# Kernel optimization log

Measured on AMD Instinct MI355X. Metric: run time of the kernel, lower is better.

The kernel has to match this reference:

```python
import jax, jax.numpy as jnp
import numpy as np

N_NODES = 10000
N_EDGES = 160000
NEG_SLOPE = 0.2  # PyG GATConv default leaky_relu slope


def gat_conv(x, src, dst, W, a_src, a_dst, b, heads, out_ch, concat, n):
    # linear projection per head: [n, heads, out_ch]
    h = (x @ W).reshape(n, heads, out_ch)
    # per-node attention logits
    al_s = jnp.sum(h * a_src, axis=-1)  # [n, heads]
    al_d = jnp.sum(h * a_dst, axis=-1)  # [n, heads]
    # per-edge score, softmax over incoming edges of each destination node
    e = jax.nn.leaky_relu(al_s[src] + al_d[dst], NEG_SLOPE)  # [E, heads]
    m = jax.ops.segment_max(e, dst, num_segments=n)
    p = jnp.exp(e - m[dst])
    s = jax.ops.segment_sum(p, dst, num_segments=n)
    alpha = p / (s[dst] + 1e-16)  # [E, heads]
    # weighted scatter-aggregate of source messages
    out = jax.ops.segment_sum(h[src] * alpha[..., None], dst, num_segments=n)
    out = out.reshape(n, heads * out_ch) if concat else out.mean(axis=1)
    return out + b


def setup_inputs() -> dict:
    key = jax.random.key(0)
    ks = jax.random.split(key, 16)
    x = jax.random.normal(ks[0], (N_NODES, 32), dtype=jnp.float32)
    edge_index = jax.random.randint(ks[1], (2, N_EDGES), 0, N_NODES, dtype=jnp.int64)

    def glorot(k, shape):
        fan = shape[0] + shape[-1]
        return jax.random.uniform(k, shape, jnp.float32, -1.0, 1.0) * jnp.sqrt(6.0 / fan)

    # layer 1: 32 -> 8 per head, 8 heads, concat -> 64
    W1 = glorot(ks[2], (32, 64))
    asrc1 = glorot(ks[3], (8, 8))
    adst1 = glorot(ks[4], (8, 8))
    b1 = jnp.zeros((64,), jnp.float32)
    # layer 2: 64 -> 64 per head, 8 heads, concat -> 512
    W2 = glorot(ks[5], (64, 512))
    asrc2 = glorot(ks[6], (8, 64))
    adst2 = glorot(ks[7], (8, 64))
    b2 = jnp.zeros((512,), jnp.float32)
    # layer 3: 512 -> 6, 1 head, no concat
    W3 = glorot(ks[8], (512, 6))
    asrc3 = glorot(ks[9], (1, 6))
    adst3 = glorot(ks[10], (1, 6))
    b3 = jnp.zeros((6,), jnp.float32)

    return dict(x=x, edge_index=edge_index,
                W1=W1, asrc1=asrc1, adst1=adst1, b1=b1,
                W2=W2, asrc2=asrc2, adst2=adst2, b2=b2,
                W3=W3, asrc3=asrc3, adst3=adst3, b3=b3)


def reference(x, edge_index, W1, asrc1, adst1, b1, W2, asrc2, adst2, b2, W3, asrc3, adst3, b3):
    n = x.shape[0]
    # PyG GATConv adds self-loops by default
    loops = jnp.arange(n, dtype=edge_index.dtype)
    src = jnp.concatenate([edge_index[0], loops])
    dst = jnp.concatenate([edge_index[1], loops])
    # dropout layers are identity in eval mode
    h = jax.nn.elu(gat_conv(x, src, dst, W1, asrc1, adst1, b1, 8, 8, True, n))
    h = jax.nn.elu(gat_conv(h, src, dst, W2, asrc2, adst2, b2, 8, 64, True, n))
    out = gat_conv(h, src, dst, W3, asrc3, adst3, b3, 1, 6, False, n)
    return out
```

## Files before the change

### kernel.cpp

```cpp
#include <hip/hip_runtime.h>
#include <hip/hip_bf16.h>
#include <math.h>


#define NEG_SLOPE 0.2f


__global__ __launch_bounds__(256) void count_deg(const int* __restrict__ ei,
                                                 int* __restrict__ deg, int E) {
  int e = blockIdx.x * blockDim.x + threadIdx.x;
  if (e < E) atomicAdd(&deg[ei[E + e]], 1);
}

__global__ __launch_bounds__(1024) void scan_k(const int* __restrict__ deg,
                                               int* __restrict__ rowptr,
                                               int* __restrict__ cursor, int n) {
  __shared__ int part[1024];
  int t = threadIdx.x;
  int chunk = (n + 1023) >> 10;
  int lo = t * chunk;
  int hi = min(lo + chunk, n);
  int s = 0;
  for (int i = lo; i < hi; ++i) s += deg[i];
  part[t] = s;
  __syncthreads();
  for (int off = 1; off < 1024; off <<= 1) {
    int v = (t >= off) ? part[t - off] : 0;
    __syncthreads();
    part[t] += v;
    __syncthreads();
  }
  int run = (t == 0) ? 0 : part[t - 1];
  for (int i = lo; i < hi; ++i) {
    rowptr[i] = run;
    cursor[i] = run;
    run += deg[i];
  }
  if (t == 1023) rowptr[n] = part[1023];
}

__global__ __launch_bounds__(256) void fill_edges(const int* __restrict__ ei,
                                                  int* __restrict__ cursor,
                                                  int* __restrict__ esrc,
                                                  int* __restrict__ edst, int E) {
  int e = blockIdx.x * blockDim.x + threadIdx.x;
  if (e < E) {
    int d = ei[E + e];
    int pos = atomicAdd(&cursor[d], 1);
    esrc[pos] = ei[e];
    edst[pos] = d;
  }
}


__global__ __launch_bounds__(512) void prep_av(const float* __restrict__ W1,
                                               const float* __restrict__ as1,
                                               const float* __restrict__ ad1,
                                               const float* __restrict__ W2,
                                               const float* __restrict__ as2,
                                               const float* __restrict__ ad2,
                                               float* __restrict__ av) {
  int t = threadIdx.x;
  if (blockIdx.x == 0) {
    if (t < 256) {
      int h = t >> 5, k = t & 31;
      float s = 0.f, d = 0.f;
#pragma unroll
      for (int c = 0; c < 8; ++c) {
        float w = W1[k * 64 + h * 8 + c];
        s += w * as1[h * 8 + c];
        d += w * ad1[h * 8 + c];
      }
      av[t] = s;
      av[256 + t] = d;
    }
  } else {
    int h = t >> 6, k = t & 63;
    float s = 0.f, d = 0.f;
#pragma unroll
    for (int c = 0; c < 64; ++c) {
      float w = W2[k * 512 + h * 64 + c];
      s += w * as2[h * 64 + c];
      d += w * ad2[h * 64 + c];
    }
    av[512 + t] = s;
    av[1024 + t] = d;
  }
}


template <int HH, int K>
__global__ __launch_bounds__(256) void logits_x(const float* __restrict__ X,
                                                const float* __restrict__ avs,
                                                const float* __restrict__ avd,
                                                float* __restrict__ als,
                                                float* __restrict__ ald,
                                                float* __restrict__ selfe, int n) {
  int idx = blockIdx.x * blockDim.x + threadIdx.x;
  if (idx >= n * HH) return;
  int node = idx / HH;
  int h = idx - node * HH;
  const float* xr = X + (size_t)node * K;
  const float* vs = avs + h * K;
  const float* vd = avd + h * K;
  float s0 = 0.f, s1 = 0.f;
#pragma unroll
  for (int k4 = 0; k4 < K / 4; ++k4) {
    float4 xv = *reinterpret_cast<const float4*>(&xr[k4 * 4]);
    float4 a = *reinterpret_cast<const float4*>(&vs[k4 * 4]);
    float4 b = *reinterpret_cast<const float4*>(&vd[k4 * 4]);
    s0 += xv.x * a.x + xv.y * a.y + xv.z * a.z + xv.w * a.w;
    s1 += xv.x * b.x + xv.y * b.y + xv.z * b.z + xv.w * b.w;
  }
  als[idx] = s0;
  ald[idx] = s1;
  float e = s0 + s1;
  selfe[idx] = e > 0.f ? e : NEG_SLOPE * e;
}


__global__ __launch_bounds__(256) void logits_h3(const float* __restrict__ HF,
                                                 const float* __restrict__ Asrc,
                                                 const float* __restrict__ Adst,
                                                 float* __restrict__ als,
                                                 float* __restrict__ ald,
                                                 float* __restrict__ selfe, int n) {
  int node = blockIdx.x * blockDim.x + threadIdx.x;
  if (node >= n) return;
  const float* f = HF + (size_t)node * 6;
  float s0 = 0.f, s1 = 0.f;
#pragma unroll
  for (int c = 0; c < 6; ++c) {
    float v = f[c];
    s0 += v * Asrc[c];
    s1 += v * Adst[c];
  }
  als[node] = s0;
  ald[node] = s1;
  float e = s0 + s1;
  selfe[node] = e > 0.f ? e : NEG_SLOPE * e;
}


template <int HH>
__global__ __launch_bounds__(256) void edge_e(const int* __restrict__ esrc,
                                              const int* __restrict__ edst,
                                              const float* __restrict__ als,
                                              const float* __restrict__ ald,
                                              float* __restrict__ evt, int E) {
  int e = blockIdx.x * blockDim.x + threadIdx.x;
  if (e >= E) return;
  int s = esrc[e], d = edst[e];
  if constexpr (HH == 8) {
    float4 s0 = *reinterpret_cast<const float4*>(&als[(size_t)s * 8]);
    float4 s1 = *reinterpret_cast<const float4*>(&als[(size_t)s * 8 + 4]);
    float4 d0 = *reinterpret_cast<const float4*>(&ald[(size_t)d * 8]);
    float4 d1 = *reinterpret_cast<const float4*>(&ald[(size_t)d * 8 + 4]);
    float v[8] = {s0.x + d0.x, s0.y + d0.y, s0.z + d0.z, s0.w + d0.w,
                  s1.x + d1.x, s1.y + d1.y, s1.z + d1.z, s1.w + d1.w};
    float4 o0, o1;
    o0.x = v[0] > 0.f ? v[0] : NEG_SLOPE * v[0];
    o0.y = v[1] > 0.f ? v[1] : NEG_SLOPE * v[1];
    o0.z = v[2] > 0.f ? v[2] : NEG_SLOPE * v[2];
    o0.w = v[3] > 0.f ? v[3] : NEG_SLOPE * v[3];
    o1.x = v[4] > 0.f ? v[4] : NEG_SLOPE * v[4];
    o1.y = v[5] > 0.f ? v[5] : NEG_SLOPE * v[5];
    o1.z = v[6] > 0.f ? v[6] : NEG_SLOPE * v[6];
    o1.w = v[7] > 0.f ? v[7] : NEG_SLOPE * v[7];
    *reinterpret_cast<float4*>(&evt[(size_t)e * 8]) = o0;
    *reinterpret_cast<float4*>(&evt[(size_t)e * 8 + 4]) = o1;
  } else {
    float v = als[s] + ald[d];
    evt[e] = v > 0.f ? v : NEG_SLOPE * v;
  }
}


template <int HH>
__global__ __launch_bounds__(256) void msum_alpha(float* __restrict__ evt,
                                                  const float* __restrict__ selfe,
                                                  const int* __restrict__ rowptr,
                                                  float* __restrict__ asel, int n) {
  int idx = blockIdx.x * blockDim.x + threadIdx.x;
  if (idx >= n * HH) return;
  int node = idx / HH;
  int h = idx - node * HH;
  int r0 = rowptr[node], r1 = rowptr[node + 1];
  float e0 = selfe[idx];
  float m = e0;
  for (int p = r0; p < r1; ++p) m = fmaxf(m, evt[(size_t)p * HH + h]);
  float s = __expf(e0 - m);
  float a0 = s;
  for (int p = r0; p < r1; ++p) s += __expf(evt[(size_t)p * HH + h] - m);
  float rs = 1.f / (s + 1e-16f);
  asel[idx] = a0 * rs;
  for (int p = r0; p < r1; ++p) {
    size_t q = (size_t)p * HH + h;
    evt[q] = __expf(evt[q] - m) * rs;
  }
}


__global__ __launch_bounds__(256) void agg1(const float* __restrict__ X,
                                            const float* __restrict__ alpha,
                                            const float* __restrict__ asel,
                                            const int* __restrict__ rowptr,
                                            const int* __restrict__ esrc,
                                            float* __restrict__ AGG, int n) {
  int node = blockIdx.x * 4 + (threadIdx.x >> 6);
  int lane = threadIdx.x & 63;
  if (node >= n) return;
  int ch = lane & 31;
  int half = lane >> 5;
  float xs = X[((unsigned)node << 5) + ch];
  float acc0 = asel[node * 8 + half * 4 + 0] * xs;
  float acc1 = asel[node * 8 + half * 4 + 1] * xs;
  float acc2 = asel[node * 8 + half * 4 + 2] * xs;
  float acc3 = asel[node * 8 + half * 4 + 3] * xs;
  int r0 = rowptr[node], r1 = rowptr[node + 1];
  int p = r0;
  for (; p + 2 <= r1; p += 2) {
    int s0 = esrc[p], s1 = esrc[p + 1];
    float xv0 = X[((unsigned)s0 << 5) + ch];
    float xv1 = X[((unsigned)s1 << 5) + ch];
    float4 a0 = *reinterpret_cast<const float4*>(&alpha[(size_t)p * 8 + half * 4]);
    float4 a1 = *reinterpret_cast<const float4*>(&alpha[(size_t)(p + 1) * 8 + half * 4]);
    acc0 += a0.x * xv0; acc1 += a0.y * xv0; acc2 += a0.z * xv0; acc3 += a0.w * xv0;
    acc0 += a1.x * xv1; acc1 += a1.y * xv1; acc2 += a1.z * xv1; acc3 += a1.w * xv1;
  }
  if (p < r1) {
    int s0 = esrc[p];
    float xv0 = X[((unsigned)s0 << 5) + ch];
    float4 a0 = *reinterpret_cast<const float4*>(&alpha[(size_t)p * 8 + half * 4]);
    acc0 += a0.x * xv0; acc1 += a0.y * xv0; acc2 += a0.z * xv0; acc3 += a0.w * xv0;
  }
  unsigned base = (unsigned)node * 256 + (unsigned)half * 128 + ch;
  AGG[base] = acc0;
  AGG[base + 32] = acc1;
  AGG[base + 64] = acc2;
  AGG[base + 96] = acc3;
}

__global__ __launch_bounds__(256) void agg2(const float* __restrict__ X,
                                            const float* __restrict__ alpha,
                                            const float* __restrict__ asel,
                                            const int* __restrict__ rowptr,
                                            const int* __restrict__ esrc,
                                            float* __restrict__ AGG, int n) {
  int node = blockIdx.x * 4 + (threadIdx.x >> 6);
  int lane = threadIdx.x & 63;
  if (node >= n) return;
  float acc[8];
  float xs = X[((unsigned)node << 6) + lane];
#pragma unroll
  for (int h = 0; h < 8; ++h) acc[h] = asel[node * 8 + h] * xs;
  int r0 = rowptr[node], r1 = rowptr[node + 1];
  int p = r0;
  for (; p + 2 <= r1; p += 2) {
    int s0 = esrc[p], s1 = esrc[p + 1];
    float xv0 = X[((unsigned)s0 << 6) + lane];
    float xv1 = X[((unsigned)s1 << 6) + lane];
    float4 a00 = *reinterpret_cast<const float4*>(&alpha[(size_t)p * 8]);
    float4 a01 = *reinterpret_cast<const float4*>(&alpha[(size_t)p * 8 + 4]);
    float4 a10 = *reinterpret_cast<const float4*>(&alpha[(size_t)(p + 1) * 8]);
    float4 a11 = *reinterpret_cast<const float4*>(&alpha[(size_t)(p + 1) * 8 + 4]);
    acc[0] += a00.x * xv0; acc[1] += a00.y * xv0;
    acc[2] += a00.z * xv0; acc[3] += a00.w * xv0;
    acc[4] += a01.x * xv0; acc[5] += a01.y * xv0;
    acc[6] += a01.z * xv0; acc[7] += a01.w * xv0;
    acc[0] += a10.x * xv1; acc[1] += a10.y * xv1;
    acc[2] += a10.z * xv1; acc[3] += a10.w * xv1;
    acc[4] += a11.x * xv1; acc[5] += a11.y * xv1;
    acc[6] += a11.z * xv1; acc[7] += a11.w * xv1;
  }
  if (p < r1) {
    int s0 = esrc[p];
    float xv0 = X[((unsigned)s0 << 6) + lane];
    float4 a00 = *reinterpret_cast<const float4*>(&alpha[(size_t)p * 8]);
    float4 a01 = *reinterpret_cast<const float4*>(&alpha[(size_t)p * 8 + 4]);
    acc[0] += a00.x * xv0; acc[1] += a00.y * xv0;
    acc[2] += a00.z * xv0; acc[3] += a00.w * xv0;
    acc[4] += a01.x * xv0; acc[5] += a01.y * xv0;
    acc[6] += a01.z * xv0; acc[7] += a01.w * xv0;
  }
  unsigned base = (unsigned)node * 512 + lane;
#pragma unroll
  for (int h = 0; h < 8; ++h) AGG[base + h * 64] = acc[h];
}


__global__ __launch_bounds__(256) void proj1(const float* __restrict__ AGG,
                                             const float* __restrict__ W1,
                                             const float* __restrict__ b1,
                                             float* __restrict__ OUT, int n) {
  int w = blockIdx.x * 4 + (threadIdx.x >> 6);
  int lane = threadIdx.x & 63;
  int node0 = w * 8;
  if (node0 >= n) return;
  int h = lane >> 3;
  float acc[8];
#pragma unroll
  for (int j = 0; j < 8; ++j) acc[j] = 0.f;
  for (int k = 0; k < 32; ++k) {
    float wv = W1[k * 64 + lane];
#pragma unroll
    for (int j = 0; j < 8; ++j) {
      int nd = min(node0 + j, n - 1);
      acc[j] += AGG[(unsigned)nd * 256 + h * 32 + k] * wv;
    }
  }
  float bv = b1[lane];
#pragma unroll
  for (int j = 0; j < 8; ++j) {
    int nd = node0 + j;
    if (nd >= n) break;
    float v = acc[j] + bv;
    v = v > 0.f ? v : expm1f(v);
    OUT[(unsigned)nd * 64 + lane] = v;
  }
}

__global__ __launch_bounds__(256) void proj2(const float* __restrict__ AGG,
                                             const float* __restrict__ W2,
                                             const float* __restrict__ b2,
                                             float* __restrict__ OUT, int n) {
  int w = blockIdx.x * 4 + (threadIdx.x >> 6);
  int lane = threadIdx.x & 63;
  int node0 = w * 4;
  if (node0 >= n) return;
  int c0 = lane * 8;
  int h = lane >> 3;
  float acc[4][8];
#pragma unroll
  for (int j = 0; j < 4; ++j)
#pragma unroll
    for (int c = 0; c < 8; ++c) acc[j][c] = 0.f;
  for (int k = 0; k < 64; ++k) {
    const float4 w0 = *reinterpret_cast<const float4*>(&W2[(size_t)k * 512 + c0]);
    const float4 w1 = *reinterpret_cast<const float4*>(&W2[(size_t)k * 512 + c0 + 4]);
#pragma unroll
    for (int j = 0; j < 4; ++j) {
      int nd = min(node0 + j, n - 1);
      float xv = AGG[(unsigned)nd * 512 + h * 64 + k];
      acc[j][0] += xv * w0.x; acc[j][1] += xv * w0.y;
      acc[j][2] += xv * w0.z; acc[j][3] += xv * w0.w;
      acc[j][4] += xv * w1.x; acc[j][5] += xv * w1.y;
      acc[j][6] += xv * w1.z; acc[j][7] += xv * w1.w;
    }
  }
  float4 bv0 = *reinterpret_cast<const float4*>(&b2[c0]);
  float4 bv1 = *reinterpret_cast<const float4*>(&b2[c0 + 4]);
#pragma unroll
  for (int j = 0; j < 4; ++j) {
    int nd = node0 + j;
    if (nd >= n) break;
    float v[8];
    v[0] = acc[j][0] + bv0.x; v[1] = acc[j][1] + bv0.y;
    v[2] = acc[j][2] + bv0.z; v[3] = acc[j][3] + bv0.w;
    v[4] = acc[j][4] + bv1.x; v[5] = acc[j][5] + bv1.y;
    v[6] = acc[j][6] + bv1.z; v[7] = acc[j][7] + bv1.w;
#pragma unroll
    for (int c = 0; c < 8; ++c) v[c] = v[c] > 0.f ? v[c] : expm1f(v[c]);
    float4* o = reinterpret_cast<float4*>(&OUT[(unsigned)nd * 512 + c0]);
    o[0] = make_float4(v[0], v[1], v[2], v[3]);
    o[1] = make_float4(v[4], v[5], v[6], v[7]);
  }
}

__global__ __launch_bounds__(64) void gemm_l3(const float* __restrict__ X,
                                              const float* __restrict__ W,
                                              float* __restrict__ H, int n) {
  int node = blockIdx.x;
  int lane = threadIdx.x;
  if (node >= n) return;
  float acc[6] = {0.f, 0.f, 0.f, 0.f, 0.f, 0.f};
  for (int k = lane; k < 512; k += 64) {
    float xv = X[(size_t)node * 512 + k];
#pragma unroll
    for (int c = 0; c < 6; ++c) acc[c] += xv * W[k * 6 + c];
  }
#pragma unroll
  for (int c = 0; c < 6; ++c) {
    float v = acc[c];
    for (int off = 32; off >= 1; off >>= 1) v += __shfl_down(v, off, 64);
    if (lane == 0) H[(size_t)node * 6 + c] = v;
  }
}

__global__ __launch_bounds__(256) void agg_l3(const float* __restrict__ HF,
                                              const float* __restrict__ alpha,
                                              const float* __restrict__ asel,
                                              const float* __restrict__ bias,
                                              const int* __restrict__ rowptr,
                                              const int* __restrict__ esrc,
                                              float* __restrict__ OUT, int n) {
  int node = blockIdx.x * 4 + (threadIdx.x >> 6);
  int lane = threadIdx.x & 63;
  if (node >= n) return;
  int ch = lane < 6 ? lane : 0;
  float acc = asel[node] * HF[(unsigned)node * 6u + ch];
  int r0 = rowptr[node], r1 = rowptr[node + 1];
  int p = r0;
  for (; p + 2 <= r1; p += 2) {
    int s0 = esrc[p], s1 = esrc[p + 1];
    float h0 = HF[(unsigned)s0 * 6u + ch];
    float h1 = HF[(unsigned)s1 * 6u + ch];
    float a0 = alpha[p], a1 = alpha[p + 1];
    acc += a0 * h0 + a1 * h1;
  }
  if (p < r1) acc += alpha[p] * HF[(unsigned)esrc[p] * 6u + ch];
  if (lane < 6) OUT[(unsigned)node * 6u + lane] = acc + bias[lane];
}


extern "C" void kernel_launch(void* const* d_in, const int* in_sizes, int n_in,
                              void* d_out, int out_size, void* d_ws, size_t ws_size,
                              hipStream_t stream) {
  const float* x     = (const float*)d_in[0];
  const int*   ei    = (const int*)d_in[1];
  const float* W1    = (const float*)d_in[2];
  const float* asrc1 = (const float*)d_in[3];
  const float* adst1 = (const float*)d_in[4];
  const float* b1    = (const float*)d_in[5];
  const float* W2    = (const float*)d_in[6];
  const float* asrc2 = (const float*)d_in[7];
  const float* adst2 = (const float*)d_in[8];
  const float* b2    = (const float*)d_in[9];
  const float* W3    = (const float*)d_in[10];
  const float* asrc3 = (const float*)d_in[11];
  const float* adst3 = (const float*)d_in[12];
  const float* b3    = (const float*)d_in[13];
  float* outf = (float*)d_out;

  const int n = in_sizes[0] / 32;
  const int E = in_sizes[1] / 2;

  char* ws = (char*)d_ws;
  size_t off = 0;
  auto alloc = [&](size_t bytes) {
    size_t o = off;
    off = (off + bytes + 255) & ~(size_t)255;
    return ws + o;
  };
  int* deg     = (int*)alloc((size_t)n * 4);
  int* rowptr  = (int*)alloc((size_t)(n + 1) * 4);
  int* cursor  = (int*)alloc((size_t)n * 4);
  int* esrc    = (int*)alloc((size_t)E * 4);
  int* edst    = (int*)alloc((size_t)E * 4);
  float* evt   = (float*)alloc((size_t)E * 8 * 4);
  float* selfe = (float*)alloc((size_t)n * 8 * 4);
  float* als   = (float*)alloc((size_t)n * 8 * 4);
  float* ald   = (float*)alloc((size_t)n * 8 * 4);
  float* asel  = (float*)alloc((size_t)n * 8 * 4);
  float* av    = (float*)alloc((size_t)1536 * 4);
  float* AGG1  = (float*)alloc((size_t)n * 256 * 4);
  float* x1    = (float*)alloc((size_t)n * 64 * 4);
  float* AGG2  = (float*)alloc((size_t)n * 512 * 4);
  float* x2    = (float*)alloc((size_t)n * 512 * 4);
  float* h3    = (float*)alloc((size_t)n * 6 * 4);

  hipMemsetAsync(deg, 0, (size_t)n * 4, stream);
  count_deg<<<(E + 255) / 256, 256, 0, stream>>>(ei, deg, E);
  scan_k<<<1, 1024, 0, stream>>>(deg, rowptr, cursor, n);
  fill_edges<<<(E + 255) / 256, 256, 0, stream>>>(ei, cursor, esrc, edst, E);
  prep_av<<<2, 512, 0, stream>>>(W1, asrc1, adst1, W2, asrc2, adst2, av);

  logits_x<8, 32><<<(n * 8 + 255) / 256, 256, 0, stream>>>(x, av, av + 256, als, ald, selfe, n);
  edge_e<8><<<(E + 255) / 256, 256, 0, stream>>>(esrc, edst, als, ald, evt, E);
  msum_alpha<8><<<(n * 8 + 255) / 256, 256, 0, stream>>>(evt, selfe, rowptr, asel, n);
  agg1<<<(n + 3) / 4, 256, 0, stream>>>(x, evt, asel, rowptr, esrc, AGG1, n);
  proj1<<<(n / 8 + 3) / 4 + 1, 256, 0, stream>>>(AGG1, W1, b1, x1, n);

  logits_x<8, 64><<<(n * 8 + 255) / 256, 256, 0, stream>>>(x1, av + 512, av + 1024, als, ald, selfe, n);
  edge_e<8><<<(E + 255) / 256, 256, 0, stream>>>(esrc, edst, als, ald, evt, E);
  msum_alpha<8><<<(n * 8 + 255) / 256, 256, 0, stream>>>(evt, selfe, rowptr, asel, n);
  agg2<<<(n + 3) / 4, 256, 0, stream>>>(x1, evt, asel, rowptr, esrc, AGG2, n);
  proj2<<<(n / 4 + 3) / 4 + 1, 256, 0, stream>>>(AGG2, W2, b2, x2, n);

  gemm_l3<<<n, 64, 0, stream>>>(x2, W3, h3, n);
  logits_h3<<<(n + 255) / 256, 256, 0, stream>>>(h3, asrc3, adst3, als, ald, selfe, n);
  edge_e<1><<<(E + 255) / 256, 256, 0, stream>>>(esrc, edst, als, ald, evt, E);
  msum_alpha<1><<<(n + 255) / 256, 256, 0, stream>>>(evt, selfe, rowptr, asel, n);
  agg_l3<<<(n + 3) / 4, 256, 0, stream>>>(h3, evt, asel, b3, rowptr, esrc, outf, n);
}
```

Measured before the change: 313.3 us.

## Fuse edge logits into wave-per-node softmax and merge small setup kernels

```diff
diff --git a/kernel.cpp b/kernel.cpp
--- a/kernel.cpp
+++ b/kernel.cpp
@@ -4,6 +4,10 @@
 
 
 #define NEG_SLOPE 0.2f
+
+__device__ __forceinline__ float lrelu(float v) {
+  return v > 0.f ? v : NEG_SLOPE * v;
+}
 
 
 __global__ __launch_bounds__(256) void count_deg(const int* __restrict__ ei,
@@ -12,56 +16,40 @@
   if (e < E) atomicAdd(&deg[ei[E + e]], 1);
 }
 
-__global__ __launch_bounds__(1024) void scan_k(const int* __restrict__ deg,
-                                               int* __restrict__ rowptr,
-                                               int* __restrict__ cursor, int n) {
-  __shared__ int part[1024];
-  int t = threadIdx.x;
-  int chunk = (n + 1023) >> 10;
-  int lo = t * chunk;
-  int hi = min(lo + chunk, n);
-  int s = 0;
-  for (int i = lo; i < hi; ++i) s += deg[i];
-  part[t] = s;
-  __syncthreads();
-  for (int off = 1; off < 1024; off <<= 1) {
-    int v = (t >= off) ? part[t - off] : 0;
-    __syncthreads();
-    part[t] += v;
-    __syncthreads();
-  }
-  int run = (t == 0) ? 0 : part[t - 1];
-  for (int i = lo; i < hi; ++i) {
-    rowptr[i] = run;
-    cursor[i] = run;
-    run += deg[i];
-  }
-  if (t == 1023) rowptr[n] = part[1023];
-}
-
-__global__ __launch_bounds__(256) void fill_edges(const int* __restrict__ ei,
-                                                  int* __restrict__ cursor,
-                                                  int* __restrict__ esrc,
-                                                  int* __restrict__ edst, int E) {
-  int e = blockIdx.x * blockDim.x + threadIdx.x;
-  if (e < E) {
-    int d = ei[E + e];
-    int pos = atomicAdd(&cursor[d], 1);
-    esrc[pos] = ei[e];
-    edst[pos] = d;
-  }
-}
-
-
-__global__ __launch_bounds__(512) void prep_av(const float* __restrict__ W1,
-                                               const float* __restrict__ as1,
-                                               const float* __restrict__ ad1,
-                                               const float* __restrict__ W2,
-                                               const float* __restrict__ as2,
-                                               const float* __restrict__ ad2,
-                                               float* __restrict__ av) {
+__global__ __launch_bounds__(1024) void scan3(const int* __restrict__ deg,
+                                              int* __restrict__ rowptr,
+                                              int* __restrict__ cursor, int n,
+                                              const float* __restrict__ W1,
+                                              const float* __restrict__ as1,
+                                              const float* __restrict__ ad1,
+                                              const float* __restrict__ W2,
+                                              const float* __restrict__ as2,
+                                              const float* __restrict__ ad2,
+                                              float* __restrict__ av) {
   int t = threadIdx.x;
   if (blockIdx.x == 0) {
+    __shared__ int part[1024];
+    int chunk = (n + 1023) >> 10;
+    int lo = t * chunk;
+    int hi = min(lo + chunk, n);
+    int s = 0;
+    for (int i = lo; i < hi; ++i) s += deg[i];
+    part[t] = s;
+    __syncthreads();
+    for (int off = 1; off < 1024; off <<= 1) {
+      int v = (t >= off) ? part[t - off] : 0;
+      __syncthreads();
+      part[t] += v;
+      __syncthreads();
+    }
+    int run = (t == 0) ? 0 : part[t - 1];
+    for (int i = lo; i < hi; ++i) {
+      rowptr[i] = run;
+      cursor[i] = run;
+      run += deg[i];
+    }
+    if (t == 1023) rowptr[n] = part[1023];
+  } else if (blockIdx.x == 1) {
     if (t < 256) {
       int h = t >> 5, k = t & 31;
       float s = 0.f, d = 0.f;
@@ -75,16 +63,29 @@
       av[256 + t] = d;
     }
   } else {
-    int h = t >> 6, k = t & 63;
-    float s = 0.f, d = 0.f;
-#pragma unroll
-    for (int c = 0; c < 64; ++c) {
-      float w = W2[k * 512 + h * 64 + c];
-      s += w * as2[h * 64 + c];
-      d += w * ad2[h * 64 + c];
-    }
-    av[512 + t] = s;
-    av[1024 + t] = d;
+    if (t < 512) {
+      int h = t >> 6, k = t & 63;
+      float s = 0.f, d = 0.f;
+#pragma unroll
+      for (int c = 0; c < 64; ++c) {
+        float w = W2[k * 512 + h * 64 + c];
+        s += w * as2[h * 64 + c];
+        d += w * ad2[h * 64 + c];
+      }
+      av[512 + t] = s;
+      av[1024 + t] = d;
+    }
+  }
+}
+
+__global__ __launch_bounds__(256) void fill_edges(const int* __restrict__ ei,
+                                                  int* __restrict__ cursor,
+                                                  int* __restrict__ esrc, int E) {
+  int e = blockIdx.x * blockDim.x + threadIdx.x;
+  if (e < E) {
+    int d = ei[E + e];
+    int pos = atomicAdd(&cursor[d], 1);
+    esrc[pos] = ei[e];
   }
 }
 
@@ -115,89 +116,78 @@
   als[idx] = s0;
   ald[idx] = s1;
   float e = s0 + s1;
-  selfe[idx] = e > 0.f ? e : NEG_SLOPE * e;
-}
-
-
-__global__ __launch_bounds__(256) void logits_h3(const float* __restrict__ HF,
-                                                 const float* __restrict__ Asrc,
-                                                 const float* __restrict__ Adst,
-                                                 float* __restrict__ als,
-                                                 float* __restrict__ ald,
-                                                 float* __restrict__ selfe, int n) {
-  int node = blockIdx.x * blockDim.x + threadIdx.x;
+  selfe[idx] = lrelu(e);
+}
+
+
+__global__ __launch_bounds__(256) void msum_alpha8(const int* __restrict__ esrc,
+                                                   const float* __restrict__ als,
+                                                   const float* __restrict__ ald,
+                                                   const float* __restrict__ selfe,
+                                                   const int* __restrict__ rowptr,
+                                                   float* __restrict__ alpha,
+                                                   float* __restrict__ asel, int n) {
+  int node = blockIdx.x * 4 + (threadIdx.x >> 6);
+  int lane = threadIdx.x & 63;
   if (node >= n) return;
-  const float* f = HF + (size_t)node * 6;
-  float s0 = 0.f, s1 = 0.f;
-#pragma unroll
-  for (int c = 0; c < 6; ++c) {
-    float v = f[c];
-    s0 += v * Asrc[c];
-    s1 += v * Adst[c];
-  }
-  als[node] = s0;
-  ald[node] = s1;
-  float e = s0 + s1;
-  selfe[node] = e > 0.f ? e : NEG_SLOPE * e;
-}
-
-
-template <int HH>
-__global__ __launch_bounds__(256) void edge_e(const int* __restrict__ esrc,
-                                              const int* __restrict__ edst,
-                                              const float* __restrict__ als,
-                                              const float* __restrict__ ald,
-                                              float* __restrict__ evt, int E) {
-  int e = blockIdx.x * blockDim.x + threadIdx.x;
-  if (e >= E) return;
-  int s = esrc[e], d = edst[e];
-  if constexpr (HH == 8) {
-    float4 s0 = *reinterpret_cast<const float4*>(&als[(size_t)s * 8]);
-    float4 s1 = *reinterpret_cast<const float4*>(&als[(size_t)s * 8 + 4]);
-    float4 d0 = *reinterpret_cast<const float4*>(&ald[(size_t)d * 8]);
-    float4 d1 = *reinterpret_cast<const float4*>(&ald[(size_t)d * 8 + 4]);
-    float v[8] = {s0.x + d0.x, s0.y + d0.y, s0.z + d0.z, s0.w + d0.w,
-                  s1.x + d1.x, s1.y + d1.y, s1.z + d1.z, s1.w + d1.w};
-    float4 o0, o1;
-    o0.x = v[0] > 0.f ? v[0] : NEG_SLOPE * v[0];
-    o0.y = v[1] > 0.f ? v[1] : NEG_SLOPE * v[1];
-    o0.z = v[2] > 0.f ? v[2] : NEG_SLOPE * v[2];
-    o0.w = v[3] > 0.f ? v[3] : NEG_SLOPE * v[3];
-    o1.x = v[4] > 0.f ? v[4] : NEG_SLOPE * v[4];
-    o1.y = v[5] > 0.f ? v[5] : NEG_SLOPE * v[5];
-    o1.z = v[6] > 0.f ? v[6] : NEG_SLOPE * v[6];
-    o1.w = v[7] > 0.f ? v[7] : NEG_SLOPE * v[7];
-    *reinterpret_cast<float4*>(&evt[(size_t)e * 8]) = o0;
-    *reinterpret_cast<float4*>(&evt[(size_t)e * 8 + 4]) = o1;
-  } else {
-    float v = als[s] + ald[d];
-    evt[e] = v > 0.f ? v : NEG_SLOPE * v;
-  }
-}
-
-
-template <int HH>
-__global__ __launch_bounds__(256) void msum_alpha(float* __restrict__ evt,
-                                                  const float* __restrict__ selfe,
-                                                  const int* __restrict__ rowptr,
-                                                  float* __restrict__ asel, int n) {
-  int idx = blockIdx.x * blockDim.x + threadIdx.x;
-  if (idx >= n * HH) return;
-  int node = idx / HH;
-  int h = idx - node * HH;
+  int i = lane >> 3;
+  int h = lane & 7;
+  float aldv = ald[node * 8 + h];
+  float e0 = selfe[node * 8 + h];
   int r0 = rowptr[node], r1 = rowptr[node + 1];
-  float e0 = selfe[idx];
+
   float m = e0;
-  for (int p = r0; p < r1; ++p) m = fmaxf(m, evt[(size_t)p * HH + h]);
-  float s = __expf(e0 - m);
-  float a0 = s;
-  for (int p = r0; p < r1; ++p) s += __expf(evt[(size_t)p * HH + h] - m);
-  float rs = 1.f / (s + 1e-16f);
-  asel[idx] = a0 * rs;
-  for (int p = r0; p < r1; ++p) {
-    size_t q = (size_t)p * HH + h;
-    evt[q] = __expf(evt[q] - m) * rs;
-  }
+  for (int p = r0 + i; p < r1; p += 8)
+    m = fmaxf(m, lrelu(als[esrc[p] * 8 + h] + aldv));
+  m = fmaxf(m, __shfl_xor(m, 8, 64));
+  m = fmaxf(m, __shfl_xor(m, 16, 64));
+  m = fmaxf(m, __shfl_xor(m, 32, 64));
+
+  float s = 0.f;
+  for (int p = r0 + i; p < r1; p += 8)
+    s += __expf(lrelu(als[esrc[p] * 8 + h] + aldv) - m);
+  s += __shfl_xor(s, 8, 64);
+  s += __shfl_xor(s, 16, 64);
+  s += __shfl_xor(s, 32, 64);
+  float a0 = __expf(e0 - m);
+  float rs = 1.f / (s + a0 + 1e-16f);
+  if (lane < 8) asel[node * 8 + lane] = a0 * rs;
+
+  for (int p = r0 + i; p < r1; p += 8)
+    alpha[(size_t)p * 8 + h] = __expf(lrelu(als[esrc[p] * 8 + h] + aldv) - m) * rs;
+}
+
+__global__ __launch_bounds__(256) void msum_alpha1(const int* __restrict__ esrc,
+                                                   const float* __restrict__ als,
+                                                   const float* __restrict__ ald,
+                                                   const float* __restrict__ selfe,
+                                                   const int* __restrict__ rowptr,
+                                                   float* __restrict__ alpha,
+                                                   float* __restrict__ asel, int n) {
+  int node = blockIdx.x * 4 + (threadIdx.x >> 6);
+  int lane = threadIdx.x & 63;
+  if (node >= n) return;
+  float aldv = ald[node];
+  float e0 = selfe[node];
+  int r0 = rowptr[node], r1 = rowptr[node + 1];
+
+  float m = e0;
+  for (int p = r0 + lane; p < r1; p += 64)
+    m = fmaxf(m, lrelu(als[esrc[p]] + aldv));
+#pragma unroll
+  for (int off = 1; off < 64; off <<= 1) m = fmaxf(m, __shfl_xor(m, off, 64));
+
+  float s = 0.f;
+  for (int p = r0 + lane; p < r1; p += 64)
+    s += __expf(lrelu(als[esrc[p]] + aldv) - m);
+#pragma unroll
+  for (int off = 1; off < 64; off <<= 1) s += __shfl_xor(s, off, 64);
+  float a0 = __expf(e0 - m);
+  float rs = 1.f / (s + a0 + 1e-16f);
+  if (lane == 0) asel[node] = a0 * rs;
+
+  for (int p = r0 + lane; p < r1; p += 64)
+    alpha[p] = __expf(lrelu(als[esrc[p]] + aldv) - m) * rs;
 }
 
 
@@ -211,59 +201,26 @@
   int lane = threadIdx.x & 63;
   if (node >= n) return;
   int ch = lane & 31;
-  int half = lane >> 5;
-  float xs = X[((unsigned)node << 5) + ch];
-  float acc0 = asel[node * 8 + half * 4 + 0] * xs;
-  float acc1 = asel[node * 8 + half * 4 + 1] * xs;
-  float acc2 = asel[node * 8 + half * 4 + 2] * xs;
-  float acc3 = asel[node * 8 + half * 4 + 3] * xs;
+  int eslot = lane >> 5;
+  float acc[8];
+  if (eslot == 0) {
+    float xs = X[((unsigned)node << 5) + ch];
+#pragma unroll
+    for (int h = 0; h < 8; ++h) acc[h] = asel[node * 8 + h] * xs;
+  } else {
+#pragma unroll
+    for (int h = 0; h < 8; ++h) acc[h] = 0.f;
+  }
   int r0 = rowptr[node], r1 = rowptr[node + 1];
-  int p = r0;
-  for (; p + 2 <= r1; p += 2) {
-    int s0 = esrc[p], s1 = esrc[p + 1];
+  int p = r0 + eslot;
+  for (; p + 2 < r1; p += 4) {
+    int s0 = esrc[p], s1 = esrc[p + 2];
     float xv0 = X[((unsigned)s0 << 5) + ch];
     float xv1 = X[((unsigned)s1 << 5) + ch];
-    float4 a0 = *reinterpret_cast<const float4*>(&alpha[(size_t)p * 8 + half * 4]);
-    float4 a1 = *reinterpret_cast<const float4*>(&alpha[(size_t)(p + 1) * 8 + half * 4]);
-    acc0 += a0.x * xv0; acc1 += a0.y * xv0; acc2 += a0.z * xv0; acc3 += a0.w * xv0;
-    acc0 += a1.x * xv1; acc1 += a1.y * xv1; acc2 += a1.z * xv1; acc3 += a1.w * xv1;
-  }
-  if (p < r1) {
-    int s0 = esrc[p];
-    float xv0 = X[((unsigned)s0 << 5) + ch];
-    float4 a0 = *reinterpret_cast<const float4*>(&alpha[(size_t)p * 8 + half * 4]);
-    acc0 += a0.x * xv0; acc1 += a0.y * xv0; acc2 += a0.z * xv0; acc3 += a0.w * xv0;
-  }
-  unsigned base = (unsigned)node * 256 + (unsigned)half * 128 + ch;
-  AGG[base] = acc0;
-  AGG[base + 32] = acc1;
-  AGG[base + 64] = acc2;
-  AGG[base + 96] = acc3;
-}
-
-__global__ __launch_bounds__(256) void agg2(const float* __restrict__ X,
-                                            const float* __restrict__ alpha,
-                                            const float* __restrict__ asel,
-                                            const int* __restrict__ rowptr,
-                                            const int* __restrict__ esrc,
-                                            float* __restrict__ AGG, int n) {
-  int node = blockIdx.x * 4 + (threadIdx.x >> 6);
-  int lane = threadIdx.x & 63;
-  if (node >= n) return;
-  float acc[8];
-  float xs = X[((unsigned)node << 6) + lane];
-#pragma unroll
-  for (int h = 0; h < 8; ++h) acc[h] = asel[node * 8 + h] * xs;
-  int r0 = rowptr[node], r1 = rowptr[node + 1];
-  int p = r0;
-  for (; p + 2 <= r1; p += 2) {
-    int s0 = esrc[p], s1 = esrc[p + 1];
-    float xv0 = X[((unsigned)s0 << 6) + lane];
-    float xv1 = X[((unsigned)s1 << 6) + lane];
     float4 a00 = *reinterpret_cast<const float4*>(&alpha[(size_t)p * 8]);
     float4 a01 = *reinterpret_cast<const float4*>(&alpha[(size_t)p * 8 + 4]);
-    float4 a10 = *reinterpret_cast<const float4*>(&alpha[(size_t)(p + 1) * 8]);
-    float4 a11 = *reinterpret_cast<const float4*>(&alpha[(size_t)(p + 1) * 8 + 4]);
+    float4 a10 = *reinterpret_cast<const float4*>(&alpha[(size_t)(p + 2) * 8]);
+    float4 a11 = *reinterpret_cast<const float4*>(&alpha[(size_t)(p + 2) * 8 + 4]);
     acc[0] += a00.x * xv0; acc[1] += a00.y * xv0;
     acc[2] += a00.z * xv0; acc[3] += a00.w * xv0;
     acc[4] += a01.x * xv0; acc[5] += a01.y * xv0;
@@ -275,13 +232,64 @@
   }
   if (p < r1) {
     int s0 = esrc[p];
-    float xv0 = X[((unsigned)s0 << 6) + lane];
+    float xv0 = X[((unsigned)s0 << 5) + ch];
     float4 a00 = *reinterpret_cast<const float4*>(&alpha[(size_t)p * 8]);
     float4 a01 = *reinterpret_cast<const float4*>(&alpha[(size_t)p * 8 + 4]);
     acc[0] += a00.x * xv0; acc[1] += a00.y * xv0;
     acc[2] += a00.z * xv0; acc[3] += a00.w * xv0;
     acc[4] += a01.x * xv0; acc[5] += a01.y * xv0;
     acc[6] += a01.z * xv0; acc[7] += a01.w * xv0;
+  }
+#pragma unroll
+  for (int h = 0; h < 8; ++h) acc[h] += __shfl_xor(acc[h], 32, 64);
+  if (eslot == 0) {
+    unsigned base = (unsigned)node * 256 + ch;
+#pragma unroll
+    for (int h = 0; h < 8; ++h) AGG[base + h * 32] = acc[h];
+  }
+}
+
+__global__ __launch_bounds__(256) void agg2(const float* __restrict__ X,
+                                            const float* __restrict__ alpha,
+                                            const float* __restrict__ asel,
+                                            const int* __restrict__ rowptr,
+                                            const int* __restrict__ esrc,
+                                            float* __restrict__ AGG, int n) {
+  int node = blockIdx.x * 4 + (threadIdx.x >> 6);
+  int lane = threadIdx.x & 63;
+  if (node >= n) return;
+  float acc[8];
+  float xs = X[((unsigned)node << 6) + lane];
+#pragma unroll
+  for (int h = 0; h < 8; ++h) acc[h] = asel[node * 8 + h] * xs;
+  int r0 = rowptr[node], r1 = rowptr[node + 1];
+  int p = r0;
+  for (; p + 4 <= r1; p += 4) {
+    int s0 = esrc[p], s1 = esrc[p + 1], s2 = esrc[p + 2], s3 = esrc[p + 3];
+    float xv0 = X[((unsigned)s0 << 6) + lane];
+    float xv1 = X[((unsigned)s1 << 6) + lane];
+    float xv2 = X[((unsigned)s2 << 6) + lane];
+    float xv3 = X[((unsigned)s3 << 6) + lane];
+#pragma unroll
+    for (int q = 0; q < 4; ++q) {
+      float xv = q == 0 ? xv0 : q == 1 ? xv1 : q == 2 ? xv2 : xv3;
+      float4 a0 = *reinterpret_cast<const float4*>(&alpha[(size_t)(p + q) * 8]);
+      float4 a1 = *reinterpret_cast<const float4*>(&alpha[(size_t)(p + q) * 8 + 4]);
+      acc[0] += a0.x * xv; acc[1] += a0.y * xv;
+      acc[2] += a0.z * xv; acc[3] += a0.w * xv;
+      acc[4] += a1.x * xv; acc[5] += a1.y * xv;
+      acc[6] += a1.z * xv; acc[7] += a1.w * xv;
+    }
+  }
+  for (; p < r1; ++p) {
+    int s0 = esrc[p];
+    float xv = X[((unsigned)s0 << 6) + lane];
+    float4 a0 = *reinterpret_cast<const float4*>(&alpha[(size_t)p * 8]);
+    float4 a1 = *reinterpret_cast<const float4*>(&alpha[(size_t)p * 8 + 4]);
+    acc[0] += a0.x * xv; acc[1] += a0.y * xv;
+    acc[2] += a0.z * xv; acc[3] += a0.w * xv;
+    acc[4] += a1.x * xv; acc[5] += a1.y * xv;
+    acc[6] += a1.z * xv; acc[7] += a1.w * xv;
   }
   unsigned base = (unsigned)node * 512 + lane;
 #pragma unroll
@@ -367,11 +375,16 @@
   }
 }
 
-__global__ __launch_bounds__(64) void gemm_l3(const float* __restrict__ X,
-                                              const float* __restrict__ W,
-                                              float* __restrict__ H, int n) {
-  int node = blockIdx.x;
-  int lane = threadIdx.x;
+__global__ __launch_bounds__(256) void gemm_l3f(const float* __restrict__ X,
+                                                const float* __restrict__ W,
+                                                const float* __restrict__ As,
+                                                const float* __restrict__ Ad,
+                                                float* __restrict__ H,
+                                                float* __restrict__ als,
+                                                float* __restrict__ ald,
+                                                float* __restrict__ selfe, int n) {
+  int node = blockIdx.x * 4 + (threadIdx.x >> 6);
+  int lane = threadIdx.x & 63;
   if (node >= n) return;
   float acc[6] = {0.f, 0.f, 0.f, 0.f, 0.f, 0.f};
   for (int k = lane; k < 512; k += 64) {
@@ -381,9 +394,21 @@
   }
 #pragma unroll
   for (int c = 0; c < 6; ++c) {
-    float v = acc[c];
-    for (int off = 32; off >= 1; off >>= 1) v += __shfl_down(v, off, 64);
-    if (lane == 0) H[(size_t)node * 6 + c] = v;
+#pragma unroll
+    for (int off = 32; off >= 1; off >>= 1)
+      acc[c] += __shfl_down(acc[c], off, 64);
+  }
+  if (lane == 0) {
+    float s0 = 0.f, s1 = 0.f;
+#pragma unroll
+    for (int c = 0; c < 6; ++c) {
+      H[(size_t)node * 6 + c] = acc[c];
+      s0 += acc[c] * As[c];
+      s1 += acc[c] * Ad[c];
+    }
+    als[node] = s0;
+    ald[node] = s1;
+    selfe[node] = lrelu(s0 + s1);
   }
 }
 
@@ -405,8 +430,7 @@
     int s0 = esrc[p], s1 = esrc[p + 1];
     float h0 = HF[(unsigned)s0 * 6u + ch];
     float h1 = HF[(unsigned)s1 * 6u + ch];
-    float a0 = alpha[p], a1 = alpha[p + 1];
-    acc += a0 * h0 + a1 * h1;
+    acc += alpha[p] * h0 + alpha[p + 1] * h1;
   }
   if (p < r1) acc += alpha[p] * HF[(unsigned)esrc[p] * 6u + ch];
   if (lane < 6) OUT[(unsigned)node * 6u + lane] = acc + bias[lane];
@@ -446,8 +470,7 @@
   int* rowptr  = (int*)alloc((size_t)(n + 1) * 4);
   int* cursor  = (int*)alloc((size_t)n * 4);
   int* esrc    = (int*)alloc((size_t)E * 4);
-  int* edst    = (int*)alloc((size_t)E * 4);
-  float* evt   = (float*)alloc((size_t)E * 8 * 4);
+  float* alpha = (float*)alloc((size_t)E * 8 * 4);
   float* selfe = (float*)alloc((size_t)n * 8 * 4);
   float* als   = (float*)alloc((size_t)n * 8 * 4);
   float* ald   = (float*)alloc((size_t)n * 8 * 4);
@@ -459,27 +482,25 @@
   float* x2    = (float*)alloc((size_t)n * 512 * 4);
   float* h3    = (float*)alloc((size_t)n * 6 * 4);
 
+  int nb4 = (n + 3) / 4;
+
   hipMemsetAsync(deg, 0, (size_t)n * 4, stream);
   count_deg<<<(E + 255) / 256, 256, 0, stream>>>(ei, deg, E);
-  scan_k<<<1, 1024, 0, stream>>>(deg, rowptr, cursor, n);
-  fill_edges<<<(E + 255) / 256, 256, 0, stream>>>(ei, cursor, esrc, edst, E);
-  prep_av<<<2, 512, 0, stream>>>(W1, asrc1, adst1, W2, asrc2, adst2, av);
+  scan3<<<3, 1024, 0, stream>>>(deg, rowptr, cursor, n,
+                                W1, asrc1, adst1, W2, asrc2, adst2, av);
+  fill_edges<<<(E + 255) / 256, 256, 0, stream>>>(ei, cursor, esrc, E);
 
   logits_x<8, 32><<<(n * 8 + 255) / 256, 256, 0, stream>>>(x, av, av + 256, als, ald, selfe, n);
-  edge_e<8><<<(E + 255) / 256, 256, 0, stream>>>(esrc, edst, als, ald, evt, E);
-  msum_alpha<8><<<(n * 8 + 255) / 256, 256, 0, stream>>>(evt, selfe, rowptr, asel, n);
-  agg1<<<(n + 3) / 4, 256, 0, stream>>>(x, evt, asel, rowptr, esrc, AGG1, n);
+  msum_alpha8<<<nb4, 256, 0, stream>>>(esrc, als, ald, selfe, rowptr, alpha, asel, n);
+  agg1<<<nb4, 256, 0, stream>>>(x, alpha, asel, rowptr, esrc, AGG1, n);
   proj1<<<(n / 8 + 3) / 4 + 1, 256, 0, stream>>>(AGG1, W1, b1, x1, n);
 
   logits_x<8, 64><<<(n * 8 + 255) / 256, 256, 0, stream>>>(x1, av + 512, av + 1024, als, ald, selfe, n);
-  edge_e<8><<<(E + 255) / 256, 256, 0, stream>>>(esrc, edst, als, ald, evt, E);
-  msum_alpha<8><<<(n * 8 + 255) / 256, 256, 0, stream>>>(evt, selfe, rowptr, asel, n);
-  agg2<<<(n + 3) / 4, 256, 0, stream>>>(x1, evt, asel, rowptr, esrc, AGG2, n);
+  msum_alpha8<<<nb4, 256, 0, stream>>>(esrc, als, ald, selfe, rowptr, alpha, asel, n);
+  agg2<<<nb4, 256, 0, stream>>>(x1, alpha, asel, rowptr, esrc, AGG2, n);
   proj2<<<(n / 4 + 3) / 4 + 1, 256, 0, stream>>>(AGG2, W2, b2, x2, n);
 
-  gemm_l3<<<n, 64, 0, stream>>>(x2, W3, h3, n);
-  logits_h3<<<(n + 255) / 256, 256, 0, stream>>>(h3, asrc3, adst3, als, ald, selfe, n);
-  edge_e<1><<<(E + 255) / 256, 256, 0, stream>>>(esrc, edst, als, ald, evt, E);
-  msum_alpha<1><<<(n + 255) / 256, 256, 0, stream>>>(evt, selfe, rowptr, asel, n);
-  agg_l3<<<(n + 3) / 4, 256, 0, stream>>>(h3, evt, asel, b3, rowptr, esrc, outf, n);
-}
+  gemm_l3f<<<nb4, 256, 0, stream>>>(x2, W3, asrc3, adst3, h3, als, ald, selfe, n);
+  msum_alpha1<<<nb4, 256, 0, stream>>>(esrc, als, ald, selfe, rowptr, alpha, asel, n);
+  agg_l3<<<nb4, 256, 0, stream>>>(h3, alpha, asel, b3, rowptr, esrc, outf, n);
+}
```

New measurement: 256.4 us. 1.22x faster.
